# Optimization experiments

Hardware: AMD Instinct MI355X
Metric: run time of the kernel (lower is better)

Reference implementation:

```python
import jax, jax.numpy as jnp
import numpy as np
from numpy.lib.stride_tricks import sliding_window_view

# Static configuration matching init_kwargs
F_, H_, W_ = 2, 32, 32          # video_shape
K = 5                            # kernel_size (odd)
HEADS, DIM_HEAD = 8, 64
N = F_ * H_ * W_                 # number of video tokens (2048)
PAD = K // 2
INNER = HEADS * DIM_HEAD         # 512


def _neighbors():
    # Flattened token index at each (f,h,w); pad with sentinel N (out of bounds -> zeros / masked)
    idx = np.arange(N, dtype=np.int32).reshape(F_, H_, W_)
    padded = np.full((F_ + 2 * PAD, H_ + 2 * PAD, W_ + 2 * PAD), N, dtype=np.int32)
    padded[PAD:PAD + F_, PAD:PAD + H_, PAD:PAD + W_] = idx
    # sliding_window_view matches unfoldNd's kernel-offset ordering (kf, kh, kw row-major)
    return sliding_window_view(padded, (K, K, K)).reshape(N, K ** 3)


NBR = jnp.asarray(_neighbors())                                   # [N, K^3]
# causal: query i attends only to neighbors with index <= i; prepend BOS column (never masked)
CAUSAL = jnp.pad(jnp.arange(N)[:, None] < NBR, ((0, 0), (1, 0)))  # [N, K^3 + 1]


def setup_inputs() -> dict:
    key = jax.random.key(0)
    k1, k2, k3 = jax.random.split(key, 3)
    return {
        "x": jax.random.normal(k1, (1, N, INNER), jnp.float32),
        "w_qkv": jax.random.normal(k2, (INNER, 3 * INNER), jnp.float32) * 0.02,
        "w_out": jax.random.normal(k3, (INNER, INNER), jnp.float32) * 0.02,
        "b_out": jnp.zeros((INNER,), jnp.float32),
    }


def reference(x, w_qkv, w_out, b_out):
    b, n, dim = x.shape            # n == N
    bh = b * HEADS
    scale = DIM_HEAD ** -0.5

    xp = jnp.pad(x, ((0, 0), (0, 1), (0, 0)))        # pad one zero token at the end: [b, n+1, dim]
    qkv = xp @ w_qkv                                  # [b, n+1, 3*inner]
    q, kk, vv = jnp.split(qkv, 3, axis=-1)

    def split_heads(t):  # 'b n (h d) -> (b h) n d'
        return t.reshape(b, n + 1, HEADS, DIM_HEAD).transpose(0, 2, 1, 3).reshape(bh, n + 1, DIM_HEAD)

    q, kk, vv = map(split_heads, (q, kk, vv))
    q = q[:, 1:] * scale                              # drop BOS query: [bh, n, d]
    k_bos, kk = kk[:, :1], kk[:, 1:]                  # BOS kv + n spatial tokens
    v_bos, vv = vv[:, :1], vv[:, 1:]

    # Append a zero row so the sentinel index N gathers zeros (== unfold's zero padding)
    zero = jnp.zeros((bh, 1, DIM_HEAD), kk.dtype)
    kw = jnp.concatenate([kk, zero], axis=1)[:, NBR]  # [bh, n, K^3, d]
    vw = jnp.concatenate([vv, zero], axis=1)[:, NBR]

    bos_k = jnp.broadcast_to(k_bos[:, None], (bh, n, 1, DIM_HEAD))
    bos_v = jnp.broadcast_to(v_bos[:, None], (bh, n, 1, DIM_HEAD))
    kw = jnp.concatenate([bos_k, kw], axis=2)         # [bh, n, K^3+1, d]
    vw = jnp.concatenate([bos_v, vw], axis=2)

    sim = jnp.einsum('bid,bijd->bij', q, kw)          # [bh, n, K^3+1]
    sim = jnp.where(CAUSAL[:n], -jnp.finfo(sim.dtype).max, sim)
    attn = jax.nn.softmax(sim, axis=-1)
    out = jnp.einsum('bij,bijd->bid', attn, vw)       # [bh, n, d]

    out = jnp.concatenate([v_bos, out], axis=1)       # BOS output = its value: [bh, n+1, d]
    out = out.reshape(b, HEADS, n + 1, DIM_HEAD).transpose(0, 2, 1, 3).reshape(b, n + 1, INNER)
    return (out @ w_out + b_out)[:, :n]
```

## Files before the change

### kernel.cpp

```cpp
#include <hip/hip_runtime.h>
#include <hip/hip_bf16.h>

#define NTOK  2048
#define INNER 512
#define KDIM  512
#define QKVP  1536

typedef __attribute__((ext_vector_type(8))) short bf16x8;
typedef __attribute__((ext_vector_type(4))) float f32x4;

__device__ __forceinline__ unsigned short f2b(float f) {
  unsigned int u = __float_as_uint(f);
  return (unsigned short)((u + 0x7FFFu + ((u >> 16) & 1u)) >> 16);
}

__device__ __forceinline__ void async_copy16(const unsigned short* g, unsigned short* l) {
  __builtin_amdgcn_global_load_lds((const __attribute__((address_space(1))) void*)g,
                                   (__attribute__((address_space(3))) void*)l, 16, 0, 0);
}

__global__ __launch_bounds__(256) void prep(const float* __restrict__ w_qkv,
                                            const float* __restrict__ w_out,
                                            const float* __restrict__ x,
                                            unsigned short* __restrict__ wqkvT,
                                            unsigned short* __restrict__ woutT,
                                            unsigned short* __restrict__ xb,
                                            int* __restrict__ glist,
                                            int* __restrict__ gcnt) {
  __shared__ float tile[32][33];
  __shared__ int list[192];
  __shared__ int cntS;
  const int tid = threadIdx.x;
  int b = blockIdx.x;

  if (b >= 1152) {
    const int i = (b - 1152) * 1024 + tid * 4;
    float4 v = *(const float4*)(x + i);
    ushort4 o;
    o.x = f2b(v.x); o.y = f2b(v.y); o.z = f2b(v.z); o.w = f2b(v.w);
    *(ushort4*)(xb + i) = o;
    return;
  }

  if (b < 1024) {
    const float* in; unsigned short* out; int K, N, bx, by;
    if (b < 768) { in = w_qkv; out = wqkvT; K = 512; N = 1536; bx = b % 48; by = b / 48; }
    else { int bb = b - 768; in = w_out; out = woutT; K = 512; N = 512; bx = bb & 15; by = bb >> 4; }
    const int k0 = by * 32, n0 = bx * 32;
    const int r = tid >> 3, c4 = (tid & 7) * 4;
    float4 v = *(const float4*)(in + (size_t)(k0 + r) * N + n0 + c4);
    tile[r][c4 + 0] = v.x; tile[r][c4 + 1] = v.y;
    tile[r][c4 + 2] = v.z; tile[r][c4 + 3] = v.w;
    __syncthreads();
    ushort4 o;
    o.x = f2b(tile[c4 + 0][r]);
    o.y = f2b(tile[c4 + 1][r]);
    o.z = f2b(tile[c4 + 2][r]);
    o.w = f2b(tile[c4 + 3][r]);
    *(ushort4*)(out + (size_t)(n0 + r) * K + k0 + c4) = o;
    return;
  }

  const int pt = b - 1024;
  const int f  = pt >> 6;
  const int hh = (pt >> 1) & 31;
  const int w0 = (pt & 1) << 4;

  if (tid < 192) list[tid] = 0x7FFFFFFF;
  if (tid == 0) { list[0] = 0; cntS = 1; }
  __syncthreads();
  if (tid >= 1 && tid <= 160) {
    int cc = tid - 1;
    int p = cc / 20, wo = cc - p * 20;
    int ff = (p < 5) ? 0 : 1;
    int h2 = hh - 2 + ((p < 5) ? p : (p - 5));
    bool ok = (p < 5) ? ((f == 1) ? (h2 >= 0 && h2 <= 31) : (p <= 2 && h2 >= 0))
                      : (f == 1 && h2 >= 0);
    if (ok) {
      bool diag = (ff == f) && (h2 == hh);
      int wlo = max(0, w0 - 2);
      int whi = min(31, diag ? (w0 + 15) : (w0 + 17));
      int w2 = wlo + wo;
      if (w2 <= whi) {
        int pos = atomicAdd(&cntS, 1);
        list[pos] = ((ff << 10) | (h2 << 5) | w2) + 1;
      }
    }
  }
  __syncthreads();
  if (tid < 192) glist[pt * 192 + tid] = list[tid];
  if (tid == 0) gcnt[pt] = cntS;
}

__global__ __launch_bounds__(256, 4) void gemm_qkv(const unsigned short* __restrict__ A,
                                                   const unsigned short* __restrict__ Bt,
                                                   unsigned short* __restrict__ C) {
  constexpr int BK = 32, N = 1536, K = 512;
  __shared__ __align__(16) unsigned short As[64 * BK];
  __shared__ __align__(16) unsigned short Bs[64 * BK];
  const int tid = threadIdx.x, lane = tid & 63, wave = tid >> 6;
  const int m0 = blockIdx.y * 64, n0 = blockIdx.x * 64;
  const int wm = (wave >> 1) * 32, wn = (wave & 1) * 32;
  const int li = tid * 8, r = li >> 5, c = li & 31;
  const int fr = lane & 15, fk = (lane >> 4) * 8;

  f32x4 acc[2][2] = {};

  for (int k0 = 0; k0 < K; k0 += BK) {
    async_copy16(A  + (size_t)(m0 + r) * K + k0 + c, &As[li]);
    async_copy16(Bt + (size_t)(n0 + r) * K + k0 + c, &Bs[li]);
    __syncthreads();
    bf16x8 af[2], bfr[2];
#pragma unroll
    for (int i = 0; i < 2; ++i) af[i] = *(const bf16x8*)&As[(wm + i * 16 + fr) * BK + fk];
#pragma unroll
    for (int j = 0; j < 2; ++j) bfr[j] = *(const bf16x8*)&Bs[(wn + j * 16 + fr) * BK + fk];
#pragma unroll
    for (int i = 0; i < 2; ++i)
#pragma unroll
      for (int j = 0; j < 2; ++j)
        acc[i][j] = __builtin_amdgcn_mfma_f32_16x16x32_bf16(af[i], bfr[j], acc[i][j], 0, 0, 0);
    __syncthreads();
  }

  const int er = (lane >> 4) * 4, ec = lane & 15;
#pragma unroll
  for (int i = 0; i < 2; ++i)
#pragma unroll
    for (int j = 0; j < 2; ++j) {
      const int col = n0 + wn + j * 16 + ec;
#pragma unroll
      for (int rr = 0; rr < 4; ++rr) {
        const int row = m0 + wm + i * 16 + er + rr;
        C[(size_t)row * N + col] = f2b(acc[i][j][rr]);
      }
    }
}

__global__ __launch_bounds__(256, 4) void gemm_out(const unsigned short* __restrict__ A,
                                                   const unsigned short* __restrict__ Bt,
                                                   const float* __restrict__ bias,
                                                   float* __restrict__ C) {
  constexpr int BK = 32, N = 512, K = 512;
  __shared__ __align__(16) unsigned short As[32 * BK];
  __shared__ __align__(16) unsigned short Bs[64 * BK];
  const int tid = threadIdx.x, lane = tid & 63, wave = tid >> 6;
  const int m0 = blockIdx.y * 32, n0 = blockIdx.x * 64;
  const int wm = (wave >> 1) * 16, wn = (wave & 1) * 32;
  const int li = tid * 8, r = li >> 5, c = li & 31;
  const int fr = lane & 15, fk = (lane >> 4) * 8;

  f32x4 acc[2] = {};

  for (int k0 = 0; k0 < K; k0 += BK) {
    if (tid < 128) async_copy16(A + (size_t)(m0 + r) * K + k0 + c, &As[li]);
    async_copy16(Bt + (size_t)(n0 + r) * K + k0 + c, &Bs[li]);
    __syncthreads();
    bf16x8 af, bfr[2];
    af = *(const bf16x8*)&As[(wm + fr) * BK + fk];
#pragma unroll
    for (int j = 0; j < 2; ++j) bfr[j] = *(const bf16x8*)&Bs[(wn + j * 16 + fr) * BK + fk];
#pragma unroll
    for (int j = 0; j < 2; ++j)
      acc[j] = __builtin_amdgcn_mfma_f32_16x16x32_bf16(af, bfr[j], acc[j], 0, 0, 0);
    __syncthreads();
  }

  const int er = (lane >> 4) * 4, ec = lane & 15;
#pragma unroll
  for (int j = 0; j < 2; ++j) {
    const int col = n0 + wn + j * 16 + ec;
    const float b = bias[col];
#pragma unroll
    for (int rr = 0; rr < 4; ++rr) {
      const int row = m0 + wm + er + rr;
      C[(size_t)row * N + col] = acc[j][rr] + b;
    }
  }
}

__global__ __launch_bounds__(256) void attn_mfma(const unsigned short* __restrict__ qkv,
                                                 const int* __restrict__ glist,
                                                 const int* __restrict__ gcnt,
                                                 unsigned short* __restrict__ O) {
  __shared__ __align__(16) int list[192];
  __shared__ __align__(16) float mOd[2][16][72];
  __shared__ float mM[2][16], mL[2][16];
  __shared__ int cntS;

  const int tid = threadIdx.x;
  const int hp = blockIdx.y;

  if (blockIdx.x == 128) {
    if (tid < 128) O[hp * 128 + tid] = qkv[1024 + hp * 128 + tid];
    return;
  }
  const int pt = blockIdx.x;
  const int f  = pt >> 6;
  const int hh = (pt >> 1) & 31;
  const int w0 = (pt & 1) << 4;
  const int base_i = (f << 10) | (hh << 5) | w0;

  if (tid < 192) list[tid] = glist[pt * 192 + tid];
  if (tid == 0) cntS = gcnt[pt];
  __syncthreads();
  const int nsub = (cntS + 15) >> 4;

  const int lane = tid & 63;
  const int wave = tid >> 6;
  const int hw   = wave >> 1;
  const int half = wave & 1;
  const int head = hp * 2 + hw;
  const int quad = lane >> 4;
  const int ec   = lane & 15;

  const int i_q = base_i + ec;
  const int tq  = min(i_q + 1, 2047);
  const unsigned short* qrow = qkv + (size_t)tq * QKVP + head * 64 + quad * 8;
  const bf16x8 qb0 = *(const bf16x8*)(qrow);
  const bf16x8 qb1 = *(const bf16x8*)(qrow + 32);

  f32x4 Od[4] = {{0,0,0,0},{0,0,0,0},{0,0,0,0},{0,0,0,0}};
  float m = -1e30f, l = 0.0f;

  for (int sub = half; sub < nsub; sub += 2) {
    const int base = sub * 16;
    const int tok_e = list[base + ec];
    const int4 tokv = *(const int4*)&list[base + quad * 4];
    const int tk[4] = {tokv.x, tokv.y, tokv.z, tokv.w};

    f32x4 S = {0, 0, 0, 0};
    {
      const int t0 = (tok_e > 2047) ? 0 : tok_e;
      const unsigned short* kr = qkv + (size_t)t0 * QKVP + 512 + head * 64 + quad * 8;
      const bf16x8 kf0 = *(const bf16x8*)(kr);
      const bf16x8 kf1 = *(const bf16x8*)(kr + 32);
      S = __builtin_amdgcn_mfma_f32_16x16x32_bf16(kf0, qb0, S, 0, 0, 0);
      S = __builtin_amdgcn_mfma_f32_16x16x32_bf16(kf1, qb1, S, 0, 0, 0);
    }

    float Sm[4];
#pragma unroll
    for (int r = 0; r < 4; ++r) {
      const int tok = tk[r];
      const int idx = tok - 1;
      const bool v = (tok == 0) ||
                     ((idx <= i_q) && ((unsigned)((idx & 31) - (w0 + ec) + 2) <= 4u));
      Sm[r] = v ? S[r] * 0.125f : -1e30f;
    }
    float mx = fmaxf(fmaxf(Sm[0], Sm[1]), fmaxf(Sm[2], Sm[3]));
    mx = fmaxf(mx, __shfl_xor(mx, 16, 64));
    mx = fmaxf(mx, __shfl_xor(mx, 32, 64));
    const float mn = fmaxf(m, mx);
    const float corr = __expf(m - mn);
    m = mn;
    const float p0 = __expf(Sm[0] - mn);
    const float p1 = __expf(Sm[1] - mn);
    const float p2 = __expf(Sm[2] - mn);
    const float p3 = __expf(Sm[3] - mn);
    float rs = (p0 + p1) + (p2 + p3);
    rs += __shfl_xor(rs, 16, 64);
    rs += __shfl_xor(rs, 32, 64);
    l = l * corr + rs;

    bf16x8 pf;
    pf[0] = (short)f2b(p0); pf[1] = (short)f2b(p1);
    pf[2] = (short)f2b(p2); pf[3] = (short)f2b(p3);
    pf[4] = 0; pf[5] = 0; pf[6] = 0; pf[7] = 0;

    const unsigned short* vp[4];
#pragma unroll
    for (int j = 0; j < 4; ++j) {
      const int tv = (tk[j] > 2047) ? 0 : tk[j];
      vp[j] = qkv + (size_t)tv * QKVP + 1024 + head * 64 + ec;
    }
#pragma unroll
    for (int dt = 0; dt < 4; ++dt) {
      bf16x8 vf;
#pragma unroll
      for (int j = 0; j < 4; ++j) vf[j] = (short)vp[j][dt * 16];
      vf[4] = 0; vf[5] = 0; vf[6] = 0; vf[7] = 0;
#pragma unroll
      for (int r = 0; r < 4; ++r) Od[dt][r] *= corr;
      Od[dt] = __builtin_amdgcn_mfma_f32_16x16x32_bf16(vf, pf, Od[dt], 0, 0, 0);
    }
  }

  if (half == 1) {
#pragma unroll
    for (int dt = 0; dt < 4; ++dt)
      *(f32x4*)&mOd[hw][ec][dt * 16 + quad * 4] = Od[dt];
    if (quad == 0) { mM[hw][ec] = m; mL[hw][ec] = l; }
  }
  __syncthreads();
  if (half == 0 && i_q <= 2046) {
    const float m1 = mM[hw][ec], l1 = mL[hw][ec];
    const float mm = fmaxf(m, m1);
    const float c0 = __expf(m - mm), c1 = __expf(m1 - mm);
    const float rl = 1.0f / (l * c0 + l1 * c1);
    unsigned short* ob = O + (size_t)(i_q + 1) * 512 + head * 64 + quad * 4;
#pragma unroll
    for (int dt = 0; dt < 4; ++dt) {
      const f32x4 o1 = *(const f32x4*)&mOd[hw][ec][dt * 16 + quad * 4];
      ushort4 u;
      u.x = f2b((Od[dt][0] * c0 + o1[0] * c1) * rl);
      u.y = f2b((Od[dt][1] * c0 + o1[1] * c1) * rl);
      u.z = f2b((Od[dt][2] * c0 + o1[2] * c1) * rl);
      u.w = f2b((Od[dt][3] * c0 + o1[3] * c1) * rl);
      *(ushort4*)(ob + dt * 16) = u;
    }
  }
}


extern "C" void kernel_launch(void* const* d_in, const int* in_sizes, int n_in,
                              void* d_out, int out_size, void* d_ws, size_t ws_size,
                              hipStream_t stream) {
  const float* x     = (const float*)d_in[0];
  const float* w_qkv = (const float*)d_in[1];
  const float* w_out = (const float*)d_in[2];
  const float* b_out = (const float*)d_in[3];
  float* out = (float*)d_out;

  char* ws = (char*)d_ws;
  unsigned short* qkvb  = (unsigned short*)(ws);
  unsigned short* wqkvT = (unsigned short*)(ws + 6291456);
  unsigned short* woutT = (unsigned short*)(ws + 7864320);
  unsigned short* Ob    = (unsigned short*)(ws + 8388608);
  unsigned short* xb    = (unsigned short*)(ws + 10485760);
  int*            glist = (int*)(ws + 12582912);
  int*            gcnt  = (int*)(ws + 12681216);

  hipLaunchKernelGGL(prep, dim3(2176), dim3(256), 0, stream,
                     w_qkv, w_out, x, wqkvT, woutT, xb, glist, gcnt);

  hipLaunchKernelGGL(gemm_qkv, dim3(24, 32), dim3(256), 0, stream, xb, wqkvT, qkvb);

  hipLaunchKernelGGL(attn_mfma, dim3(129, 4), dim3(256), 0, stream, qkvb, glist, gcnt, Ob);

  hipLaunchKernelGGL(gemm_out, dim3(8, 64), dim3(256), 0, stream, Ob, woutT, b_out, out);
}
```

Before: 96.37 us.

## Stage V rows through LDS with vector loads and split each head over four waves

The attention kernel now gives one head per block (grid y goes from 4 to 8) and spreads the key sub-tiles over four waves instead of two, merging four partial softmax states at the end. V rows are loaded with 16-byte vector loads, the same way K is loaded, and written to a per-wave LDS tile; the MFMA operand is then built from LDS instead of from scattered 2-byte global loads. The goal is to replace many uncoalesced scalar global reads with coalesced ones and to raise parallelism. The cost is more LDS traffic, a wider final reduction, and the BOS rows being written per head rather than per head pair.

```diff
diff --git a/kernel.cpp b/kernel.cpp
--- a/kernel.cpp
+++ b/kernel.cpp
@@ -179,20 +179,21 @@
   }
 }
 
-__global__ __launch_bounds__(256) void attn_mfma(const unsigned short* __restrict__ qkv,
-                                                 const int* __restrict__ glist,
-                                                 const int* __restrict__ gcnt,
-                                                 unsigned short* __restrict__ O) {
+__global__ __launch_bounds__(256, 4) void attn_mfma(const unsigned short* __restrict__ qkv,
+                                                    const int* __restrict__ glist,
+                                                    const int* __restrict__ gcnt,
+                                                    unsigned short* __restrict__ O) {
   __shared__ __align__(16) int list[192];
-  __shared__ __align__(16) float mOd[2][16][72];
-  __shared__ float mM[2][16], mL[2][16];
+  __shared__ __align__(16) unsigned short Vlds[4][16 * 72];
+  __shared__ __align__(16) float mOd[3][16][72];
+  __shared__ float mM[3][16], mL[3][16];
   __shared__ int cntS;
 
-  const int tid = threadIdx.x;
-  const int hp = blockIdx.y;
+  const int tid  = threadIdx.x;
+  const int head = blockIdx.y;
 
   if (blockIdx.x == 128) {
-    if (tid < 128) O[hp * 128 + tid] = qkv[1024 + hp * 128 + tid];
+    if (tid < 64) O[head * 64 + tid] = qkv[1024 + head * 64 + tid];
     return;
   }
   const int pt = blockIdx.x;
@@ -208,9 +209,6 @@
 
   const int lane = tid & 63;
   const int wave = tid >> 6;
-  const int hw   = wave >> 1;
-  const int half = wave & 1;
-  const int head = hp * 2 + hw;
   const int quad = lane >> 4;
   const int ec   = lane & 15;
 
@@ -220,24 +218,31 @@
   const bf16x8 qb0 = *(const bf16x8*)(qrow);
   const bf16x8 qb1 = *(const bf16x8*)(qrow + 32);
 
+  unsigned short* vbuf = &Vlds[wave][0];
+
   f32x4 Od[4] = {{0,0,0,0},{0,0,0,0},{0,0,0,0},{0,0,0,0}};
   float m = -1e30f, l = 0.0f;
 
-  for (int sub = half; sub < nsub; sub += 2) {
+  for (int sub = wave; sub < nsub; sub += 4) {
     const int base = sub * 16;
     const int tok_e = list[base + ec];
     const int4 tokv = *(const int4*)&list[base + quad * 4];
     const int tk[4] = {tokv.x, tokv.y, tokv.z, tokv.w};
 
+    const int t0 = (tok_e > 2047) ? 0 : tok_e;
+    const unsigned short* kr = qkv + (size_t)t0 * QKVP + 512 + head * 64 + quad * 8;
+    const unsigned short* vr = qkv + (size_t)t0 * QKVP + 1024 + head * 64 + quad * 8;
+    const bf16x8 kf0 = *(const bf16x8*)(kr);
+    const bf16x8 kf1 = *(const bf16x8*)(kr + 32);
+    const bf16x8 vs0 = *(const bf16x8*)(vr);
+    const bf16x8 vs1 = *(const bf16x8*)(vr + 32);
+
     f32x4 S = {0, 0, 0, 0};
-    {
-      const int t0 = (tok_e > 2047) ? 0 : tok_e;
-      const unsigned short* kr = qkv + (size_t)t0 * QKVP + 512 + head * 64 + quad * 8;
-      const bf16x8 kf0 = *(const bf16x8*)(kr);
-      const bf16x8 kf1 = *(const bf16x8*)(kr + 32);
-      S = __builtin_amdgcn_mfma_f32_16x16x32_bf16(kf0, qb0, S, 0, 0, 0);
-      S = __builtin_amdgcn_mfma_f32_16x16x32_bf16(kf1, qb1, S, 0, 0, 0);
-    }
+    S = __builtin_amdgcn_mfma_f32_16x16x32_bf16(kf0, qb0, S, 0, 0, 0);
+    S = __builtin_amdgcn_mfma_f32_16x16x32_bf16(kf1, qb1, S, 0, 0, 0);
+
+    *(bf16x8*)&vbuf[ec * 72 + quad * 8]      = vs0;
+    *(bf16x8*)&vbuf[ec * 72 + 32 + quad * 8] = vs1;
 
     float Sm[4];
 #pragma unroll
@@ -268,17 +273,11 @@
     pf[2] = (short)f2b(p2); pf[3] = (short)f2b(p3);
     pf[4] = 0; pf[5] = 0; pf[6] = 0; pf[7] = 0;
 
-    const unsigned short* vp[4];
-#pragma unroll
-    for (int j = 0; j < 4; ++j) {
-      const int tv = (tk[j] > 2047) ? 0 : tk[j];
-      vp[j] = qkv + (size_t)tv * QKVP + 1024 + head * 64 + ec;
-    }
 #pragma unroll
     for (int dt = 0; dt < 4; ++dt) {
       bf16x8 vf;
 #pragma unroll
-      for (int j = 0; j < 4; ++j) vf[j] = (short)vp[j][dt * 16];
+      for (int j = 0; j < 4; ++j) vf[j] = (short)vbuf[(quad * 4 + j) * 72 + dt * 16 + ec];
       vf[4] = 0; vf[5] = 0; vf[6] = 0; vf[7] = 0;
 #pragma unroll
       for (int r = 0; r < 4; ++r) Od[dt][r] *= corr;
@@ -286,27 +285,32 @@
     }
   }
 
-  if (half == 1) {
+  if (wave > 0) {
 #pragma unroll
     for (int dt = 0; dt < 4; ++dt)
-      *(f32x4*)&mOd[hw][ec][dt * 16 + quad * 4] = Od[dt];
-    if (quad == 0) { mM[hw][ec] = m; mL[hw][ec] = l; }
+      *(f32x4*)&mOd[wave - 1][ec][dt * 16 + quad * 4] = Od[dt];
+    if (quad == 0) { mM[wave - 1][ec] = m; mL[wave - 1][ec] = l; }
   }
   __syncthreads();
-  if (half == 0 && i_q <= 2046) {
-    const float m1 = mM[hw][ec], l1 = mL[hw][ec];
-    const float mm = fmaxf(m, m1);
-    const float c0 = __expf(m - mm), c1 = __expf(m1 - mm);
-    const float rl = 1.0f / (l * c0 + l1 * c1);
+  if (wave == 0 && i_q <= 2046) {
+    const float m1 = mM[0][ec], m2 = mM[1][ec], m3 = mM[2][ec];
+    const float mm = fmaxf(fmaxf(m, m1), fmaxf(m2, m3));
+    const float c0 = __expf(m - mm);
+    const float c1 = __expf(m1 - mm);
+    const float c2 = __expf(m2 - mm);
+    const float c3 = __expf(m3 - mm);
+    const float rl = 1.0f / (l * c0 + mL[0][ec] * c1 + mL[1][ec] * c2 + mL[2][ec] * c3);
     unsigned short* ob = O + (size_t)(i_q + 1) * 512 + head * 64 + quad * 4;
 #pragma unroll
     for (int dt = 0; dt < 4; ++dt) {
-      const f32x4 o1 = *(const f32x4*)&mOd[hw][ec][dt * 16 + quad * 4];
+      const f32x4 o1 = *(const f32x4*)&mOd[0][ec][dt * 16 + quad * 4];
+      const f32x4 o2 = *(const f32x4*)&mOd[1][ec][dt * 16 + quad * 4];
+      const f32x4 o3 = *(const f32x4*)&mOd[2][ec][dt * 16 + quad * 4];
       ushort4 u;
-      u.x = f2b((Od[dt][0] * c0 + o1[0] * c1) * rl);
-      u.y = f2b((Od[dt][1] * c0 + o1[1] * c1) * rl);
-      u.z = f2b((Od[dt][2] * c0 + o1[2] * c1) * rl);
-      u.w = f2b((Od[dt][3] * c0 + o1[3] * c1) * rl);
+      u.x = f2b((Od[dt][0] * c0 + o1[0] * c1 + o2[0] * c2 + o3[0] * c3) * rl);
+      u.y = f2b((Od[dt][1] * c0 + o1[1] * c1 + o2[1] * c2 + o3[1] * c3) * rl);
+      u.z = f2b((Od[dt][2] * c0 + o1[2] * c1 + o2[2] * c2 + o3[2] * c3) * rl);
+      u.w = f2b((Od[dt][3] * c0 + o1[3] * c1 + o2[3] * c2 + o3[3] * c3) * rl);
       *(ushort4*)(ob + dt * 16) = u;
     }
   }
@@ -336,7 +340,7 @@
 
   hipLaunchKernelGGL(gemm_qkv, dim3(24, 32), dim3(256), 0, stream, xb, wqkvT, qkvb);
 
-  hipLaunchKernelGGL(attn_mfma, dim3(129, 4), dim3(256), 0, stream, qkvb, glist, gcnt, Ob);
+  hipLaunchKernelGGL(attn_mfma, dim3(129, 8), dim3(256), 0, stream, qkvb, glist, gcnt, Ob);
 
   hipLaunchKernelGGL(gemm_out, dim3(8, 64), dim3(256), 0, stream, Ob, woutT, b_out, out);
 }
```

Measured after the change: 93.54 us. 1.03x faster.
